# Performance work log

Hardware: AMD Instinct MI355X
Metric: run time of the kernel (lower is better)

The kernel has to match this reference:

```python
import jax, jax.numpy as jnp
import numpy as np

B, N, CZ, D = 1, 1024, 128, 6
LN_EPS = 1e-5
MASK_VALUE = 1000000.0  # float32 path in the original


def setup_inputs() -> dict:
    key = jax.random.key(0)
    k1, k2 = jax.random.split(key)
    pair = jax.random.normal(k1, (B, N, N, CZ), dtype=jnp.float32)
    seq_index = jnp.broadcast_to(jnp.arange(N, dtype=jnp.int64), (B, N))
    ln_scale = jnp.ones((CZ,), dtype=jnp.float32)
    ln_bias = jnp.zeros((CZ,), dtype=jnp.float32)
    W = jax.random.normal(k2, (CZ, D), dtype=jnp.float32) * (1.0 / np.sqrt(CZ))
    b = jnp.zeros((D,), dtype=jnp.float32)
    return {"pair": pair, "seq_index": seq_index, "ln_scale": ln_scale,
            "ln_bias": ln_bias, "W": W, "b": b}


def reference(pair, seq_index, ln_scale, ln_bias, W, b):
    # LayerNorm over channel dim
    mu = jnp.mean(pair, axis=-1, keepdims=True)
    var = jnp.mean(jnp.square(pair - mu), axis=-1, keepdims=True)
    h = (pair - mu) * jax.lax.rsqrt(var + LN_EPS) * ln_scale + ln_bias
    # Linear -> [B, N, N, D]
    x = jnp.einsum('bijc,cd->bijd', h, W) + b
    # symmetrize over (i, j)
    x = (x + jnp.swapaxes(x, -3, -2)) * 0.5
    # sequence-separation mask: |i - j| > 3
    si = seq_index[..., :, None]
    sj = seq_index[..., None, :]
    m = jnp.abs(si - sj) > 3  # [B, N, N]
    x = jnp.where(m[..., None], x, -MASK_VALUE)
    # padded triple log_softmax: row (axis -2), column (axis -3), channel (axis -1)
    l = x.shape[-2]
    u = jnp.zeros(x.shape[:-3] + (l, 1, D), dtype=x.dtype)
    v = jnp.zeros(x.shape[:-3] + (1, l, D), dtype=x.dtype)
    w = jnp.zeros(x.shape[:-3] + (l, l, 1), dtype=x.dtype)
    row = jax.nn.log_softmax(jnp.concatenate((u, x), axis=-2), axis=-2)[..., 1:, :]
    col = jax.nn.log_softmax(jnp.concatenate((v, x), axis=-3), axis=-3)[..., 1:, :, :]
    chn = jax.nn.log_softmax(jnp.concatenate((w, x), axis=-1), axis=-1)[..., 1:]
    return row + col + 2.0 * chn
```

## Files before the change

kernel.cpp:

```cpp
#include <hip/hip_runtime.h>

#define NN 1024
#define NP (NN * NN)
#define NBLK 1024
#define NGRP (NBLK * 16)

typedef float f32x4 __attribute__((ext_vector_type(4)));

__device__ __forceinline__ f32x4 ntld(const float* p) {
  return __builtin_nontemporal_load((const f32x4*)p);
}

#define DPP_ADD_STAGE(v, ctrl)                                               \
  {                                                                          \
    const int _t = __builtin_amdgcn_update_dpp(                              \
        0, __float_as_int(v), (ctrl), 0xf, 0xf, true);                       \
    (v) += __int_as_float(_t);                                               \
  }

__global__ __launch_bounds__(256) void k_ln_gemv(
    const float* __restrict__ pairp, const float* __restrict__ gamma,
    const float* __restrict__ beta, const float* __restrict__ W,
    const float* __restrict__ bvec, float* __restrict__ xout)
{
  const int l = threadIdx.x & 15;
  const int group = blockIdx.x * 16 + (threadIdx.x >> 4);

  float ug[8][6], apart[6] = {0, 0, 0, 0, 0, 0}, bpart[6] = {0, 0, 0, 0, 0, 0};
#pragma unroll
  for (int k = 0; k < 2; ++k)
#pragma unroll
    for (int m = 0; m < 4; ++m) {
      const int c = 4 * l + 64 * k + m;
      const int idx = 4 * k + m;
      const float ga = gamma[c], be = beta[c];
#pragma unroll
      for (int d = 0; d < 6; ++d) {
        const float w = W[c * 6 + d];
        ug[idx][d] = ga * w;
        apart[d] += ga * w;
        bpart[d] += be * w;
      }
    }
#pragma unroll
  for (int d = 0; d < 6; ++d)
#pragma unroll
    for (int m = 1; m <= 8; m <<= 1) {
      apart[d] += __shfl_xor(apart[d], m);
      bpart[d] += __shfl_xor(bpart[d], m);
    }
  const float vA = (l == 0) ? apart[0] : (l == 1) ? apart[1] : (l == 2) ? apart[2]
                  : (l == 3) ? apart[3] : (l == 4) ? apart[4] : apart[5];
  float vB = (l == 0) ? bpart[0] : (l == 1) ? bpart[1] : (l == 2) ? bpart[2]
            : (l == 3) ? bpart[3] : (l == 4) ? bpart[4] : bpart[5];
  if (l < 6) vB += bvec[l];

  size_t p = 2 * (size_t)group;
  const float* bp = pairp + p * 128 + 4 * l;
  f32x4 a0 = ntld(bp), b0 = ntld(bp + 64);
  f32x4 a1 = ntld(bp + 128), b1 = ntld(bp + 192);

  for (int it = 0; it < 32; ++it) {
    const size_t pn = p + 2 * NGRP;
    f32x4 na0, nb0, na1, nb1;
    if (it != 31) {
      const float* nbp = pairp + pn * 128 + 4 * l;
      na0 = ntld(nbp); nb0 = ntld(nbp + 64);
      na1 = ntld(nbp + 128); nb1 = ntld(nbp + 192);
    }

    const float xv0[8] = {a0.x, a0.y, a0.z, a0.w, b0.x, b0.y, b0.z, b0.w};
    const float xv1[8] = {a1.x, a1.y, a1.z, a1.w, b1.x, b1.y, b1.z, b1.w};
    float r[16];
#pragma unroll
    for (int k = 0; k < 16; ++k) r[k] = 0.f;
#pragma unroll
    for (int k = 0; k < 8; ++k) {
      r[0] += xv0[k];
      r[1] = fmaf(xv0[k], xv0[k], r[1]);
      r[8] += xv1[k];
      r[9] = fmaf(xv1[k], xv1[k], r[9]);
#pragma unroll
      for (int d = 0; d < 6; ++d) {
        r[2 + d] = fmaf(xv0[k], ug[k][d], r[2 + d]);
        r[10 + d] = fmaf(xv1[k], ug[k][d], r[10 + d]);
      }
    }
#pragma unroll
    for (int k = 0; k < 16; ++k) DPP_ADD_STAGE(r[k], 0xB1);
#pragma unroll
    for (int k = 0; k < 16; ++k) DPP_ADD_STAGE(r[k], 0x4E);
#pragma unroll
    for (int k = 0; k < 16; ++k) DPP_ADD_STAGE(r[k], 0x141);
#pragma unroll
    for (int k = 0; k < 16; ++k) DPP_ADD_STAGE(r[k], 0x140);

    if (l < 6) {
      const float mu0 = r[0] * (1.f / 128.f);
      const float var0 = r[1] * (1.f / 128.f) - mu0 * mu0;
      const float rstd0 = rsqrtf(var0 + 1e-5f);
      const float vg0 = (l == 0) ? r[2] : (l == 1) ? r[3] : (l == 2) ? r[4]
                       : (l == 3) ? r[5] : (l == 4) ? r[6] : r[7];
      xout[p * 6 + l] = fmaf(rstd0, vg0 - mu0 * vA, vB);

      const float mu1 = r[8] * (1.f / 128.f);
      const float var1 = r[9] * (1.f / 128.f) - mu1 * mu1;
      const float rstd1 = rsqrtf(var1 + 1e-5f);
      const float vg1 = (l == 0) ? r[10] : (l == 1) ? r[11] : (l == 2) ? r[12]
                       : (l == 3) ? r[13] : (l == 4) ? r[14] : r[15];
      xout[(p + 1) * 6 + l] = fmaf(rstd1, vg1 - mu1 * vA, vB);
    }
    p = pn;
    a0 = na0; b0 = nb0; a1 = na1; b1 = nb1;
  }
}

__global__ __launch_bounds__(256) void k_sym(
    const float* __restrict__ x, const int* __restrict__ seq,
    float* __restrict__ xs, float* __restrict__ rowsum)
{
  const int J = blockIdx.x, I = blockIdx.y;
  const int tid = threadIdx.x;
  __shared__ float M[32 * 193];

  const float* mb = x + ((size_t)(J * 32) * NN + I * 32) * 6;
  for (int k = tid; k < 1536; k += 256) {
    const int m = k / 48, f = k % 48;
    const float4 v = *(const float4*)(mb + (size_t)m * (NN * 6) + f * 4);
    float* dst = &M[m * 193 + f * 4];
    dst[0] = v.x; dst[1] = v.y; dst[2] = v.z; dst[3] = v.w;
  }
  __syncthreads();

  float es[4][6];
#pragma unroll
  for (int q = 0; q < 4; ++q) {
    const int e = tid + 256 * q;
    const int r = e >> 5, c = e & 31;
    const int i = I * 32 + r, j = J * 32 + c;
    const int dd = seq[i] - seq[j];
    const bool far = (dd > 3) || (dd < -3);
    const float* own = x + ((size_t)i * NN + j) * 6;
    const float2 o0 = *(const float2*)(own);
    const float2 o1 = *(const float2*)(own + 2);
    const float2 o2 = *(const float2*)(own + 4);
    const float* mr = &M[c * 193 + r * 6];
    float v[6];
    v[0] = far ? 0.5f * (o0.x + mr[0]) : -1000000.f;
    v[1] = far ? 0.5f * (o0.y + mr[1]) : -1000000.f;
    v[2] = far ? 0.5f * (o1.x + mr[2]) : -1000000.f;
    v[3] = far ? 0.5f * (o1.y + mr[3]) : -1000000.f;
    v[4] = far ? 0.5f * (o2.x + mr[4]) : -1000000.f;
    v[5] = far ? 0.5f * (o2.y + mr[5]) : -1000000.f;
    float* op = xs + ((size_t)i * NN + j) * 6;
    *(float2*)(op) = make_float2(v[0], v[1]);
    *(float2*)(op + 2) = make_float2(v[2], v[3]);
    *(float2*)(op + 4) = make_float2(v[4], v[5]);
#pragma unroll
    for (int d = 0; d < 6; ++d) es[q][d] = __expf(v[d]);
  }

#pragma unroll
  for (int q = 0; q < 4; ++q)
#pragma unroll
    for (int d = 0; d < 6; ++d)
#pragma unroll
      for (int m = 1; m <= 16; m <<= 1) es[q][d] += __shfl_xor(es[q][d], m);

  if ((tid & 31) == 0) {
    const int w = tid >> 5;
#pragma unroll
    for (int q = 0; q < 4; ++q) {
      const int i = I * 32 + w + 8 * q;
#pragma unroll
      for (int d = 0; d < 6; ++d) atomicAdd(&rowsum[i * 6 + d], es[q][d]);
    }
  }
}

__global__ __launch_bounds__(256) void k_lse(
    const float* __restrict__ rowsum, float* __restrict__ lse)
{
  const int k = blockIdx.x * 256 + threadIdx.x;
  if (k < NN * 6) lse[k] = logf(1.0f + rowsum[k]);
}

__global__ __launch_bounds__(256) void k_out(
    float* __restrict__ out, const float* __restrict__ lse)
{
  const int p = blockIdx.x * 256 + threadIdx.x;
  const int i = p >> 10;
  const int j = p & (NN - 1);

  float* a = out + (size_t)p * 6;
  const float2 a0 = *(const float2*)(a);
  const float2 a1 = *(const float2*)(a + 2);
  const float2 a2 = *(const float2*)(a + 4);
  const float v[6] = {a0.x, a0.y, a1.x, a1.y, a2.x, a2.y};

  float ssum = 0.f;
#pragma unroll
  for (int d = 0; d < 6; ++d) ssum += __expf(v[d]);
  const float lc2 = 2.f * logf(1.f + ssum);

  const float* li = lse + i * 6;
  const float* lj = lse + j * 6;
  float o[6];
#pragma unroll
  for (int d = 0; d < 6; ++d) o[d] = 4.f * v[d] - li[d] - lj[d] - lc2;

  *(float2*)(a) = make_float2(o[0], o[1]);
  *(float2*)(a + 2) = make_float2(o[2], o[3]);
  *(float2*)(a + 4) = make_float2(o[4], o[5]);
}

extern "C" void kernel_launch(void* const* d_in, const int* in_sizes, int n_in,
                              void* d_out, int out_size, void* d_ws, size_t ws_size,
                              hipStream_t stream) {
  const float* pairp = (const float*)d_in[0];
  const int* seq = (const int*)d_in[1];
  const float* gamma = (const float*)d_in[2];
  const float* beta = (const float*)d_in[3];
  const float* W = (const float*)d_in[4];
  const float* bvec = (const float*)d_in[5];
  float* out = (float*)d_out;

  float* x = (float*)d_ws;
  float* rowsum = x + (size_t)NP * 6;
  float* lse = rowsum + NN * 6;

  hipMemsetAsync(rowsum, 0, NN * 6 * sizeof(float), stream);
  k_ln_gemv<<<NBLK, 256, 0, stream>>>(pairp, gamma, beta, W, bvec, x);
  k_sym<<<dim3(32, 32), 256, 0, stream>>>(x, seq, out, rowsum);
  k_lse<<<(NN * 6 + 255) / 256, 256, 0, stream>>>(rowsum, lse);
  k_out<<<NP / 256, 256, 0, stream>>>(out, lse);
}
```

Before: 151.1 us.

## Fuse symmetrize, LSE and output into one cooperative grid-synced kernel

Replaces the sym, lse and out kernels with a single cooperative kernel. Each block processes two 32x32 tiles, keeps the masked values and channel exp sums in registers, accumulates row sums atomically, waits on a grid-wide sync, then computes the log terms and writes the final output. The memset is folded into the first kernel. This removes a full reread and rewrite of the 24MB intermediate output and two kernel launches. The cost is the grid sync, higher register pressure, and a fallback path if the cooperative launch fails.

```diff
diff --git a/kernel.cpp b/kernel.cpp
--- a/kernel.cpp
+++ b/kernel.cpp
@@ -1,4 +1,7 @@
 #include <hip/hip_runtime.h>
+#include <hip/hip_cooperative_groups.h>
+
+namespace cg = cooperative_groups;
 
 #define NN 1024
 #define NP (NN * NN)
@@ -21,8 +24,13 @@
 __global__ __launch_bounds__(256) void k_ln_gemv(
     const float* __restrict__ pairp, const float* __restrict__ gamma,
     const float* __restrict__ beta, const float* __restrict__ W,
-    const float* __restrict__ bvec, float* __restrict__ xout)
-{
+    const float* __restrict__ bvec, float* __restrict__ xout,
+    float* __restrict__ rowsum)
+{
+  if (blockIdx.x == 0) {
+    for (int k = threadIdx.x; k < NN * 6; k += 256) rowsum[k] = 0.f;
+  }
+
   const int l = threadIdx.x & 15;
   const int group = blockIdx.x * 16 + (threadIdx.x >> 4);
 
@@ -112,6 +120,122 @@
     }
     p = pn;
     a0 = na0; b0 = nb0; a1 = na1; b1 = nb1;
+  }
+}
+
+#define DO_TILE(VOFF, JT)                                                     \
+  {                                                                           \
+    __syncthreads();                                                          \
+    const float* mb = x + ((size_t)((JT) * 32) * NN + I * 32) * 6;            \
+    for (int k = tid; k < 1536; k += 256) {                                   \
+      const int m = k / 48, f = k % 48;                                       \
+      const float4 v4 = *(const float4*)(mb + (size_t)m * (NN * 6) + f * 4);  \
+      float* dst = &M[m * 193 + f * 4];                                       \
+      dst[0] = v4.x; dst[1] = v4.y; dst[2] = v4.z; dst[3] = v4.w;             \
+    }                                                                         \
+    __syncthreads();                                                          \
+    _Pragma("unroll")                                                         \
+    for (int q = 0; q < 4; ++q) {                                             \
+      const int e = tid + 256 * q;                                            \
+      const int r = e >> 5, c = e & 31;                                       \
+      const int i = I * 32 + r, j = (JT) * 32 + c;                            \
+      const int dd = seq[i] - seq[j];                                         \
+      const bool far = (dd > 3) || (dd < -3);                                 \
+      const float* own = x + ((size_t)i * NN + j) * 6;                        \
+      const float2 o0 = *(const float2*)(own);                                \
+      const float2 o1 = *(const float2*)(own + 2);                            \
+      const float2 o2 = *(const float2*)(own + 4);                            \
+      const float* mr = &M[c * 193 + r * 6];                                  \
+      v[(VOFF) + q][0] = far ? 0.5f * (o0.x + mr[0]) : -1000000.f;            \
+      v[(VOFF) + q][1] = far ? 0.5f * (o0.y + mr[1]) : -1000000.f;            \
+      v[(VOFF) + q][2] = far ? 0.5f * (o1.x + mr[2]) : -1000000.f;            \
+      v[(VOFF) + q][3] = far ? 0.5f * (o1.y + mr[3]) : -1000000.f;            \
+      v[(VOFF) + q][4] = far ? 0.5f * (o2.x + mr[4]) : -1000000.f;            \
+      v[(VOFF) + q][5] = far ? 0.5f * (o2.y + mr[5]) : -1000000.f;            \
+      float ss = 0.f;                                                         \
+      _Pragma("unroll")                                                       \
+      for (int d = 0; d < 6; ++d) {                                           \
+        const float e_ = __expf(v[(VOFF) + q][d]);                            \
+        esum[q][d] += e_;                                                     \
+        ss += e_;                                                             \
+      }                                                                       \
+      ssum[(VOFF) + q] = ss;                                                  \
+    }                                                                         \
+  }
+
+__global__ __launch_bounds__(256, 4) void k_down2(
+    const float* __restrict__ x, const int* __restrict__ seq,
+    float* __restrict__ rowsum, float* __restrict__ out)
+{
+  cg::grid_group grid = cg::this_grid();
+  const int Jp = blockIdx.x, I = blockIdx.y;
+  const int J0 = 2 * Jp, J1 = 2 * Jp + 1;
+  const int tid = threadIdx.x;
+  __shared__ float M[32 * 193];
+  __shared__ float LSI[192], LSJ0[192], LSJ1[192];
+
+  float v[8][6], ssum[8], esum[4][6];
+#pragma unroll
+  for (int q = 0; q < 4; ++q)
+#pragma unroll
+    for (int d = 0; d < 6; ++d) esum[q][d] = 0.f;
+
+  DO_TILE(0, J0)
+  DO_TILE(4, J1)
+
+#pragma unroll
+  for (int q = 0; q < 4; ++q)
+#pragma unroll
+    for (int d = 0; d < 6; ++d)
+#pragma unroll
+      for (int m = 1; m <= 16; m <<= 1) esum[q][d] += __shfl_xor(esum[q][d], m);
+
+  if ((tid & 31) == 0) {
+    const int w = tid >> 5;
+#pragma unroll
+    for (int q = 0; q < 4; ++q) {
+      const int i = I * 32 + w + 8 * q;
+#pragma unroll
+      for (int d = 0; d < 6; ++d) atomicAdd(&rowsum[i * 6 + d], esum[q][d]);
+    }
+  }
+
+  grid.sync();
+
+  for (int k = tid; k < 576; k += 256) {
+    if (k < 192) LSI[k] = logf(1.f + rowsum[I * 192 + k]);
+    else if (k < 384) LSJ0[k - 192] = logf(1.f + rowsum[J0 * 192 + (k - 192)]);
+    else LSJ1[k - 384] = logf(1.f + rowsum[J1 * 192 + (k - 384)]);
+  }
+  __syncthreads();
+
+#pragma unroll
+  for (int q = 0; q < 4; ++q) {
+    const int e = tid + 256 * q;
+    const int r = e >> 5, c = e & 31;
+    const int i = I * 32 + r;
+    {
+      const float lc2 = 2.f * logf(1.f + ssum[q]);
+      float o[6];
+#pragma unroll
+      for (int d = 0; d < 6; ++d)
+        o[d] = 4.f * v[q][d] - LSI[r * 6 + d] - LSJ0[c * 6 + d] - lc2;
+      float* op = out + ((size_t)i * NN + (J0 * 32 + c)) * 6;
+      *(float2*)(op) = make_float2(o[0], o[1]);
+      *(float2*)(op + 2) = make_float2(o[2], o[3]);
+      *(float2*)(op + 4) = make_float2(o[4], o[5]);
+    }
+    {
+      const float lc2 = 2.f * logf(1.f + ssum[4 + q]);
+      float o[6];
+#pragma unroll
+      for (int d = 0; d < 6; ++d)
+        o[d] = 4.f * v[4 + q][d] - LSI[r * 6 + d] - LSJ1[c * 6 + d] - lc2;
+      float* op = out + ((size_t)i * NN + (J1 * 32 + c)) * 6;
+      *(float2*)(op) = make_float2(o[0], o[1]);
+      *(float2*)(op + 2) = make_float2(o[2], o[3]);
+      *(float2*)(op + 4) = make_float2(o[4], o[5]);
+    }
   }
 }
 
@@ -229,9 +353,15 @@
   float* rowsum = x + (size_t)NP * 6;
   float* lse = rowsum + NN * 6;
 
-  hipMemsetAsync(rowsum, 0, NN * 6 * sizeof(float), stream);
-  k_ln_gemv<<<NBLK, 256, 0, stream>>>(pairp, gamma, beta, W, bvec, x);
-  k_sym<<<dim3(32, 32), 256, 0, stream>>>(x, seq, out, rowsum);
-  k_lse<<<(NN * 6 + 255) / 256, 256, 0, stream>>>(rowsum, lse);
-  k_out<<<NP / 256, 256, 0, stream>>>(out, lse);
-}
+  k_ln_gemv<<<NBLK, 256, 0, stream>>>(pairp, gamma, beta, W, bvec, x, rowsum);
+
+  const float* xc = x;
+  void* kargs[] = {(void*)&xc, (void*)&seq, (void*)&rowsum, (void*)&out};
+  hipError_t err = hipLaunchCooperativeKernel(
+      (const void*)k_down2, dim3(16, 32), dim3(256), kargs, 0, stream);
+  if (err != hipSuccess) {
+    k_sym<<<dim3(32, 32), 256, 0, stream>>>(x, seq, out, rowsum);
+    k_lse<<<(NN * 6 + 255) / 256, 256, 0, stream>>>(rowsum, lse);
+    k_out<<<NP / 256, 256, 0, stream>>>(out, lse);
+  }
+}
```

New measurement: 193.2 us. +27.9%, slower.

## Store intermediates in bf16, pair symmetric tiles, fuse lse into output kernel

Applied to the files above, without the earlier changes.

Stores the projected pair activations and the partial output in bf16 instead of fp32, roughly halving intermediate traffic. The symmetrize kernel now handles each (I,J)/(J,I) tile pair in one block over a triangular grid, so each tile is read once. It also precomputes the channel log-softmax term. The memset and lse kernel are folded into the other kernels, which removes launches. Rounding to bf16 adds precision loss in the output.

```diff
diff --git a/kernel.cpp b/kernel.cpp
--- a/kernel.cpp
+++ b/kernel.cpp
@@ -9,6 +9,14 @@
 
 __device__ __forceinline__ f32x4 ntld(const float* p) {
   return __builtin_nontemporal_load((const f32x4*)p);
+}
+
+__device__ __forceinline__ ushort bfr(float f) {
+  uint u = __float_as_uint(f);
+  return (ushort)((u + 0x7fffu + ((u >> 16) & 1u)) >> 16);
+}
+__device__ __forceinline__ float ubf(uint u) {
+  return __uint_as_float(u << 16);
 }
 
 #define DPP_ADD_STAGE(v, ctrl)                                               \
@@ -21,8 +29,13 @@
 __global__ __launch_bounds__(256) void k_ln_gemv(
     const float* __restrict__ pairp, const float* __restrict__ gamma,
     const float* __restrict__ beta, const float* __restrict__ W,
-    const float* __restrict__ bvec, float* __restrict__ xout)
-{
+    const float* __restrict__ bvec, ushort* __restrict__ xout,
+    float* __restrict__ rowsum)
+{
+  if (blockIdx.x == 0) {
+    for (int k = threadIdx.x; k < NN * 6; k += 256) rowsum[k] = 0.f;
+  }
+
   const int l = threadIdx.x & 15;
   const int group = blockIdx.x * 16 + (threadIdx.x >> 4);
 
@@ -101,117 +114,140 @@
       const float rstd0 = rsqrtf(var0 + 1e-5f);
       const float vg0 = (l == 0) ? r[2] : (l == 1) ? r[3] : (l == 2) ? r[4]
                        : (l == 3) ? r[5] : (l == 4) ? r[6] : r[7];
-      xout[p * 6 + l] = fmaf(rstd0, vg0 - mu0 * vA, vB);
+      xout[p * 6 + l] = bfr(fmaf(rstd0, vg0 - mu0 * vA, vB));
 
       const float mu1 = r[8] * (1.f / 128.f);
       const float var1 = r[9] * (1.f / 128.f) - mu1 * mu1;
       const float rstd1 = rsqrtf(var1 + 1e-5f);
       const float vg1 = (l == 0) ? r[10] : (l == 1) ? r[11] : (l == 2) ? r[12]
                        : (l == 3) ? r[13] : (l == 4) ? r[14] : r[15];
-      xout[(p + 1) * 6 + l] = fmaf(rstd1, vg1 - mu1 * vA, vB);
+      xout[(p + 1) * 6 + l] = bfr(fmaf(rstd1, vg1 - mu1 * vA, vB));
     }
     p = pn;
     a0 = na0; b0 = nb0; a1 = na1; b1 = nb1;
   }
 }
 
-__global__ __launch_bounds__(256) void k_sym(
-    const float* __restrict__ x, const int* __restrict__ seq,
-    float* __restrict__ xs, float* __restrict__ rowsum)
-{
-  const int J = blockIdx.x, I = blockIdx.y;
-  const int tid = threadIdx.x;
-  __shared__ float M[32 * 193];
-
-  const float* mb = x + ((size_t)(J * 32) * NN + I * 32) * 6;
-  for (int k = tid; k < 1536; k += 256) {
-    const int m = k / 48, f = k % 48;
-    const float4 v = *(const float4*)(mb + (size_t)m * (NN * 6) + f * 4);
-    float* dst = &M[m * 193 + f * 4];
-    dst[0] = v.x; dst[1] = v.y; dst[2] = v.z; dst[3] = v.w;
-  }
-  __syncthreads();
-
+__device__ __forceinline__ void do_tile(
+    const float* __restrict__ Mr, const float* __restrict__ Mc,
+    int rowBand, int colBand, const int* __restrict__ seq,
+    ushort* __restrict__ t, float* __restrict__ rowsum, int tid)
+{
   float es[4][6];
 #pragma unroll
   for (int q = 0; q < 4; ++q) {
     const int e = tid + 256 * q;
     const int r = e >> 5, c = e & 31;
-    const int i = I * 32 + r, j = J * 32 + c;
+    const int i = rowBand + r, j = colBand + c;
     const int dd = seq[i] - seq[j];
     const bool far = (dd > 3) || (dd < -3);
-    const float* own = x + ((size_t)i * NN + j) * 6;
-    const float2 o0 = *(const float2*)(own);
-    const float2 o1 = *(const float2*)(own + 2);
-    const float2 o2 = *(const float2*)(own + 4);
-    const float* mr = &M[c * 193 + r * 6];
-    float v[6];
-    v[0] = far ? 0.5f * (o0.x + mr[0]) : -1000000.f;
-    v[1] = far ? 0.5f * (o0.y + mr[1]) : -1000000.f;
-    v[2] = far ? 0.5f * (o1.x + mr[2]) : -1000000.f;
-    v[3] = far ? 0.5f * (o1.y + mr[3]) : -1000000.f;
-    v[4] = far ? 0.5f * (o2.x + mr[4]) : -1000000.f;
-    v[5] = far ? 0.5f * (o2.y + mr[5]) : -1000000.f;
-    float* op = xs + ((size_t)i * NN + j) * 6;
-    *(float2*)(op) = make_float2(v[0], v[1]);
-    *(float2*)(op + 2) = make_float2(v[2], v[3]);
-    *(float2*)(op + 4) = make_float2(v[4], v[5]);
-#pragma unroll
-    for (int d = 0; d < 6; ++d) es[q][d] = __expf(v[d]);
-  }
-
+    const float* mr = &Mr[r * 193 + c * 6];
+    const float* mc = &Mc[c * 193 + r * 6];
+    float xs[6], chs = 0.f;
+#pragma unroll
+    for (int d = 0; d < 6; ++d) {
+      xs[d] = far ? 0.5f * (mr[d] + mc[d]) : -1000000.f;
+      es[q][d] = __expf(xs[d]);
+      chs += es[q][d];
+    }
+    const float c2 = 2.f * logf(1.f + chs);
+    uint w0 = (uint)bfr(4.f * xs[0] - c2) | ((uint)bfr(4.f * xs[1] - c2) << 16);
+    uint w1 = (uint)bfr(4.f * xs[2] - c2) | ((uint)bfr(4.f * xs[3] - c2) << 16);
+    uint w2 = (uint)bfr(4.f * xs[4] - c2) | ((uint)bfr(4.f * xs[5] - c2) << 16);
+    uint* tp = (uint*)(t + ((size_t)i * NN + j) * 6);
+    tp[0] = w0; tp[1] = w1; tp[2] = w2;
+  }
 #pragma unroll
   for (int q = 0; q < 4; ++q)
 #pragma unroll
     for (int d = 0; d < 6; ++d)
 #pragma unroll
       for (int m = 1; m <= 16; m <<= 1) es[q][d] += __shfl_xor(es[q][d], m);
-
   if ((tid & 31) == 0) {
     const int w = tid >> 5;
 #pragma unroll
     for (int q = 0; q < 4; ++q) {
-      const int i = I * 32 + w + 8 * q;
+      const int i = rowBand + w + 8 * q;
 #pragma unroll
       for (int d = 0; d < 6; ++d) atomicAdd(&rowsum[i * 6 + d], es[q][d]);
     }
   }
 }
 
-__global__ __launch_bounds__(256) void k_lse(
-    const float* __restrict__ rowsum, float* __restrict__ lse)
-{
-  const int k = blockIdx.x * 256 + threadIdx.x;
-  if (k < NN * 6) lse[k] = logf(1.0f + rowsum[k]);
-}
-
-__global__ __launch_bounds__(256) void k_out(
-    float* __restrict__ out, const float* __restrict__ lse)
-{
-  const int p = blockIdx.x * 256 + threadIdx.x;
-  const int i = p >> 10;
-  const int j = p & (NN - 1);
-
-  float* a = out + (size_t)p * 6;
-  const float2 a0 = *(const float2*)(a);
-  const float2 a1 = *(const float2*)(a + 2);
-  const float2 a2 = *(const float2*)(a + 4);
-  const float v[6] = {a0.x, a0.y, a1.x, a1.y, a2.x, a2.y};
-
-  float ssum = 0.f;
-#pragma unroll
-  for (int d = 0; d < 6; ++d) ssum += __expf(v[d]);
-  const float lc2 = 2.f * logf(1.f + ssum);
-
-  const float* li = lse + i * 6;
-  const float* lj = lse + j * 6;
+__global__ __launch_bounds__(256) void k_sym2(
+    const ushort* __restrict__ x, const int* __restrict__ seq,
+    ushort* __restrict__ t, float* __restrict__ rowsum)
+{
+  const int b = blockIdx.x;
+  int I = (int)((sqrtf(8.f * b + 1.f) - 1.f) * 0.5f);
+  while ((I + 1) * (I + 2) / 2 <= b) ++I;
+  while (I * (I + 1) / 2 > b) --I;
+  const int J = b - I * (I + 1) / 2;
+  const int tid = threadIdx.x;
+
+  __shared__ float M1[32 * 193];
+  __shared__ float M2[32 * 193];
+
+  for (int k = tid; k < 768; k += 256) {
+    const int m = k / 24, f = (k % 24) * 8;
+    {
+      const uint4 raw = *(const uint4*)(x + ((size_t)(I * 32 + m) * NN + J * 32) * 6 + f);
+      float* dst = &M1[m * 193 + f];
+      dst[0] = ubf(raw.x & 0xffff); dst[1] = ubf(raw.x >> 16);
+      dst[2] = ubf(raw.y & 0xffff); dst[3] = ubf(raw.y >> 16);
+      dst[4] = ubf(raw.z & 0xffff); dst[5] = ubf(raw.z >> 16);
+      dst[6] = ubf(raw.w & 0xffff); dst[7] = ubf(raw.w >> 16);
+    }
+    if (I != J) {
+      const uint4 raw = *(const uint4*)(x + ((size_t)(J * 32 + m) * NN + I * 32) * 6 + f);
+      float* dst = &M2[m * 193 + f];
+      dst[0] = ubf(raw.x & 0xffff); dst[1] = ubf(raw.x >> 16);
+      dst[2] = ubf(raw.y & 0xffff); dst[3] = ubf(raw.y >> 16);
+      dst[4] = ubf(raw.z & 0xffff); dst[5] = ubf(raw.z >> 16);
+      dst[6] = ubf(raw.w & 0xffff); dst[7] = ubf(raw.w >> 16);
+    }
+  }
+  __syncthreads();
+
+  if (I != J) {
+    do_tile(M1, M2, I * 32, J * 32, seq, t, rowsum, tid);
+    do_tile(M2, M1, J * 32, I * 32, seq, t, rowsum, tid);
+  } else {
+    do_tile(M1, M1, I * 32, J * 32, seq, t, rowsum, tid);
+  }
+}
+
+__global__ __launch_bounds__(256) void k_out2(
+    const ushort* __restrict__ t, const float* __restrict__ rowsum,
+    float* __restrict__ out)
+{
+  const int b = blockIdx.x;
+  const int i = b >> 2;
+  const int j = ((b & 3) << 8) + threadIdx.x;
+
+  __shared__ float LSI[6];
+  if (threadIdx.x < 6) LSI[threadIdx.x] = logf(1.f + rowsum[i * 6 + threadIdx.x]);
+  __syncthreads();
+
+  float lj[6];
+#pragma unroll
+  for (int d = 0; d < 6; ++d) lj[d] = logf(1.f + rowsum[j * 6 + d]);
+
+  const size_t p = (size_t)i * NN + j;
+  const uint* tp = (const uint*)(t + p * 6);
+  const uint w0 = tp[0], w1 = tp[1], w2 = tp[2];
   float o[6];
-#pragma unroll
-  for (int d = 0; d < 6; ++d) o[d] = 4.f * v[d] - li[d] - lj[d] - lc2;
-
-  *(float2*)(a) = make_float2(o[0], o[1]);
-  *(float2*)(a + 2) = make_float2(o[2], o[3]);
-  *(float2*)(a + 4) = make_float2(o[4], o[5]);
+  o[0] = ubf(w0 & 0xffff) - LSI[0] - lj[0];
+  o[1] = ubf(w0 >> 16)    - LSI[1] - lj[1];
+  o[2] = ubf(w1 & 0xffff) - LSI[2] - lj[2];
+  o[3] = ubf(w1 >> 16)    - LSI[3] - lj[3];
+  o[4] = ubf(w2 & 0xffff) - LSI[4] - lj[4];
+  o[5] = ubf(w2 >> 16)    - LSI[5] - lj[5];
+
+  float* op = out + p * 6;
+  *(float2*)(op) = make_float2(o[0], o[1]);
+  *(float2*)(op + 2) = make_float2(o[2], o[3]);
+  *(float2*)(op + 4) = make_float2(o[4], o[5]);
 }
 
 extern "C" void kernel_launch(void* const* d_in, const int* in_sizes, int n_in,
@@ -225,13 +261,11 @@
   const float* bvec = (const float*)d_in[5];
   float* out = (float*)d_out;
 
-  float* x = (float*)d_ws;
-  float* rowsum = x + (size_t)NP * 6;
-  float* lse = rowsum + NN * 6;
-
-  hipMemsetAsync(rowsum, 0, NN * 6 * sizeof(float), stream);
-  k_ln_gemv<<<NBLK, 256, 0, stream>>>(pairp, gamma, beta, W, bvec, x);
-  k_sym<<<dim3(32, 32), 256, 0, stream>>>(x, seq, out, rowsum);
-  k_lse<<<(NN * 6 + 255) / 256, 256, 0, stream>>>(rowsum, lse);
-  k_out<<<NP / 256, 256, 0, stream>>>(out, lse);
-}
+  ushort* x = (ushort*)d_ws;
+  ushort* t = x + (size_t)NP * 6;
+  float* rowsum = (float*)(t + (size_t)NP * 6);
+
+  k_ln_gemv<<<NBLK, 256, 0, stream>>>(pairp, gamma, beta, W, bvec, x, rowsum);
+  k_sym2<<<528, 256, 0, stream>>>(x, seq, t, rowsum);
+  k_out2<<<NP / 256, 256, 0, stream>>>(t, rowsum, out);
+}
```

After: 133.5 us. 1.13x faster.
